# Kernel tuning notes

Hardware: AMD Instinct MI355X
Metric: run time of the kernel (lower is better)

Reference implementation:

```python
import jax, jax.numpy as jnp
import numpy as np

H = 256  # hidden size (hardcoded in module)
F_IN = 10  # input features (hardcoded via x.view(..., 10))


def _lstm_cell(x, h, c, w_ih, w_hh, b_ih, b_hh):
    # PyTorch gate order: i, f, g, o. gates: [B, 4H]
    gates = x @ w_ih.T + h @ w_hh.T + b_ih + b_hh
    i, f, g, o = jnp.split(gates, 4, axis=-1)
    c_new = jax.nn.sigmoid(f) * c + jax.nn.sigmoid(i) * jnp.tanh(g)
    h_new = jax.nn.sigmoid(o) * jnp.tanh(c_new)
    return h_new, c_new


def setup_inputs() -> dict:
    key = jax.random.key(0)
    ks = jax.random.split(key, 13)
    B, T = 512, 1024
    s = 0.05
    return {
        "x": jax.random.normal(ks[0], (B, T, F_IN), dtype=jnp.float32),
        "w_ih0": jax.random.normal(ks[1], (4 * H, F_IN), dtype=jnp.float32) * s,
        "w_hh0": jax.random.normal(ks[2], (4 * H, H), dtype=jnp.float32) * s,
        "b_ih0": jax.random.normal(ks[3], (4 * H,), dtype=jnp.float32) * s,
        "b_hh0": jax.random.normal(ks[4], (4 * H,), dtype=jnp.float32) * s,
        "w_ih1": jax.random.normal(ks[5], (4 * H, H), dtype=jnp.float32) * s,
        "w_hh1": jax.random.normal(ks[6], (4 * H, H), dtype=jnp.float32) * s,
        "b_ih1": jax.random.normal(ks[7], (4 * H,), dtype=jnp.float32) * s,
        "b_hh1": jax.random.normal(ks[8], (4 * H,), dtype=jnp.float32) * s,
        "adv_w1": jax.random.normal(ks[9], (H, H), dtype=jnp.float32) * s,
        "adv_b1": jax.random.normal(ks[10], (H,), dtype=jnp.float32) * s,
        "adv_w2": jax.random.normal(ks[11], (1, H), dtype=jnp.float32) * s,
        "adv_b2": jax.random.normal(ks[12], (1,), dtype=jnp.float32) * s,
    }


def reference(x, w_ih0, w_hh0, b_ih0, b_hh0, w_ih1, w_hh1, b_ih1, b_hh1,
              adv_w1, adv_b1, adv_w2, adv_b2):
    B, T, _ = x.shape
    h0 = jnp.zeros((B, H), dtype=x.dtype)

    def step(carry, x_t):
        h1, c1, h2, c2 = carry
        h1, c1 = _lstm_cell(x_t, h1, c1, w_ih0, w_hh0, b_ih0, b_hh0)
        h2, c2 = _lstm_cell(h1, h2, c2, w_ih1, w_hh1, b_ih1, b_hh1)
        return (h1, c1, h2, c2), h2

    xs = jnp.swapaxes(x, 0, 1)  # [T, B, F_IN]
    _, hs = jax.lax.scan(step, (h0, h0, h0, h0), xs)  # hs: [T, B, H]

    # advantage MLP head applied per-timestep
    hidden = jax.nn.relu(jnp.einsum('tbh,oh->tbo', hs, adv_w1) + adv_b1)
    scores = jnp.einsum('tbh,oh->tbo', hidden, adv_w2) + adv_b2  # [T, B, 1]

    # Faithful to torch.cat(outputs).view(B, -1): flatten TIME-major, then
    # reinterpret as [B, T] (mixes batch and time when B != T).
    flat = scores.reshape(-1)            # time-major flat buffer [T*B]
    mixed = flat.reshape(B, T)
    advantage = jax.nn.softmax(mixed, axis=1)
    return advantage.reshape(-1)
```

## Files before the change

### kernel.cpp

```cpp
#include <hip/hip_runtime.h>
#include <cstdint>
#include <cstddef>

#define Tn 1024
#define Bn 512
#define Hn 256

#define H1S 264
#define H2S 264
#define WHS 264
#define GWS 20

#define H1_OFF  0
#define H2_OFF  (H1_OFF + 32*H1S*2)
#define XB_OFF  (H2_OFF + 32*H2S*2)
#define WH_OFF  (XB_OFF + 2*32*16*2)
#define GW_OFF  (WH_OFF + 16*WHS*2)
#define B1_OFF  (GW_OFF + 8*16*GWS*4)
#define B2_OFF  (B1_OFF + 64*4)
#define BH_OFF  (B2_OFF + 64*4)
#define W2H_OFF (BH_OFF + 16*4)
#define LDS_TOTAL 90112

#define SCORES_OFF 0
#define H1G_OFF  (2*1024*1024)
#define H2G_OFF  (3*1024*1024)
#define FLAG_OFF (4*1024*1024)
#define WS_USED  (4*1024*1024 + 8192)

typedef _Float16 v4h __attribute__((ext_vector_type(4)));
typedef float    v4f __attribute__((ext_vector_type(4)));
typedef unsigned int u32x4 __attribute__((ext_vector_type(4)));
typedef unsigned long long u64;

__device__ inline float sigm(float x){ return 1.0f/(1.0f + __expf(-x)); }
__device__ inline float tanh_f(float x){ return 1.0f - 2.0f/(1.0f + __expf(2.0f*x)); }

__device__ inline v4h cvt4(float4 a){
    v4h f; f[0]=(_Float16)a.x; f[1]=(_Float16)a.y; f[2]=(_Float16)a.z; f[3]=(_Float16)a.w;
    return f;
}

__device__ inline void poll64(const int* tags, int tgt){
    int idx = threadIdx.x & 63;
    while (true){
        int t = __hip_atomic_load(&tags[idx], __ATOMIC_RELAXED, __HIP_MEMORY_SCOPE_AGENT);
        if (__ballot(t < tgt) == 0ull) break;
        __builtin_amdgcn_s_sleep(1);
    }
}

#define LADDR(oo) ( (size_t)(((oo)>>9)*528 + ((oo)&511)) )
__device__ __forceinline__ void stage_tile(const char* gbase, char* lbase, int t){
    u32x4 q0,q1,q2,q3;
    const char* p0 = gbase + t*16;
    const char* p1 = p0 + 4096;
    const char* p2 = p0 + 8192;
    const char* p3 = p0 + 12288;
    asm volatile("global_load_dwordx4 %0, %1, off sc0 sc1" : "=v"(q0) : "v"(p0));
    asm volatile("global_load_dwordx4 %0, %1, off sc0 sc1" : "=v"(q1) : "v"(p1));
    asm volatile("global_load_dwordx4 %0, %1, off sc0 sc1" : "=v"(q2) : "v"(p2));
    asm volatile("global_load_dwordx4 %0, %1, off sc0 sc1" : "=v"(q3) : "v"(p3));
    asm volatile("s_waitcnt vmcnt(0)"
                 : "+v"(q0), "+v"(q1), "+v"(q2), "+v"(q3) :: "memory");
    const int o = t*16;
    *(u32x4*)(lbase + LADDR(o))         = q0;
    *(u32x4*)(lbase + LADDR(o + 4096))  = q1;
    *(u32x4*)(lbase + LADDR(o + 8192))  = q2;
    *(u32x4*)(lbase + LADDR(o + 12288)) = q3;
}

__device__ __forceinline__ void lstm_ew_publish(v4f acc, float* gw, const float* bs,
                                                int n, float& c, _Float16* dst,
                                                int ln15, int ln4)
{
    #pragma unroll
    for (int r = 0; r < 4; ++r) gw[(ln4*4 + r)*GWS + ln15] = acc[r];
    asm volatile("s_waitcnt lgkmcnt(0)" ::: "memory");
    v4f g4 = *(const v4f*)(gw + ln15*GWS + ln4*4);
    asm volatile("s_waitcnt lgkmcnt(0)" ::: "memory");
    v4f bb = *(const v4f*)(bs + n*16 + ln4*4);
    float gi = sigm(g4.x + bb.x), gf = sigm(g4.y + bb.y);
    float gg = tanh_f(g4.z + bb.z), go = sigm(g4.w + bb.w);
    c = gf*c + gi*gg;
    float hn = go * tanh_f(c);
    union { _Float16 h; unsigned short u; } cvt; cvt.h = (_Float16)hn;
    unsigned v32 = cvt.u;
    unsigned p16 = (unsigned)__shfl_xor((int)v32, 16, 64);
    unsigned lo32 = v32 | (p16 << 16);
    unsigned hi32 = (unsigned)__shfl_xor((int)lo32, 32, 64);
    if (ln4 == 0){
        u64 pk = (u64)lo32 | ((u64)hi32 << 32);
        __hip_atomic_store((u64*)dst, pk, __ATOMIC_RELAXED, __HIP_MEMORY_SCOPE_AGENT);
    }
}

__global__ __launch_bounds__(512)
void lstm_pipe(const float* __restrict__ x,
               const float* __restrict__ w_ih0, const float* __restrict__ w_hh0,
               const float* __restrict__ b_ih0, const float* __restrict__ b_hh0,
               const float* __restrict__ w_ih1, const float* __restrict__ w_hh1,
               const float* __restrict__ b_ih1, const float* __restrict__ b_hh1,
               const float* __restrict__ adv_w1, const float* __restrict__ adv_b1,
               const float* __restrict__ adv_w2,
               float* __restrict__ scores, _Float16* __restrict__ h1g,
               _Float16* __restrict__ h2g, int* __restrict__ flags)
{
    extern __shared__ char smem[];
    _Float16* H1l = (_Float16*)(smem + H1_OFF);
    _Float16* H2l = (_Float16*)(smem + H2_OFF);
    _Float16* XBp = (_Float16*)(smem + XB_OFF);
    _Float16* WHl = (_Float16*)(smem + WH_OFF);
    float* gatesc = (float*)(smem + GW_OFF);
    float* b1s    = (float*)(smem + B1_OFF);
    float* b2s    = (float*)(smem + B2_OFF);
    float* bhs    = (float*)(smem + BH_OFF);
    float* w2hs   = (float*)(smem + W2H_OFF);

    const int tid  = threadIdx.x;
    const int lane = tid & 63;
    const int wv   = tid >> 6;
    const int ln15 = lane & 15;
    const int ln4  = lane >> 4;
    const int rt = blockIdx.x >> 4;
    const int us = blockIdx.x & 15;
    const int r0 = rt * 32;
    const int u0 = us * 16;
    const int eng = wv >> 2;
    const int wq  = wv & 3;
    const int m   = wq >> 1;
    const int n0  = (wq & 1) * 2;

    int* tags1 = flags;
    int* tags2 = flags + 1024;

    const int N0i = n0*16 + ln15;
    const int R0 = (N0i & 3)*256 + u0 + (N0i >> 2);
    const int N1i = N0i + 16;
    const int R1 = (N1i & 3)*256 + u0 + (N1i >> 2);
    v4h W[64];
    if (eng == 0){
        #pragma unroll
        for (int t = 0; t < 2; ++t){
            const int R = t ? R1 : R0;
            v4h f;
            #pragma unroll
            for (int j = 0; j < 4; ++j){
                int c = ln4*4 + j;
                f[j] = (_Float16)((c < 10) ? w_ih0[R*10 + c] : 0.f);
            }
            W[t] = f;
        }
        #pragma unroll
        for (int k = 0; k < 16; ++k){
            float4 a0 = *(const float4*)(w_hh0 + (size_t)R0*256 + k*16 + ln4*4);
            float4 a1 = *(const float4*)(w_hh0 + (size_t)R1*256 + k*16 + ln4*4);
            W[2+k]  = cvt4(a0);
            W[18+k] = cvt4(a1);
        }
    } else {
        #pragma unroll
        for (int k = 0; k < 16; ++k){
            float4 a0 = *(const float4*)(w_ih1 + (size_t)R0*256 + k*16 + ln4*4);
            float4 a1 = *(const float4*)(w_ih1 + (size_t)R1*256 + k*16 + ln4*4);
            float4 b0 = *(const float4*)(w_hh1 + (size_t)R0*256 + k*16 + ln4*4);
            float4 b1 = *(const float4*)(w_hh1 + (size_t)R1*256 + k*16 + ln4*4);
            W[k]    = cvt4(a0);
            W[16+k] = cvt4(a1);
            W[32+k] = cvt4(b0);
            W[48+k] = cvt4(b1);
        }
    }

    for (int idx = tid; idx < 16*WHS; idx += 512){
        int n = idx / WHS, c = idx - n*WHS;
        float v = (c < 256) ? adv_w1[(u0+n)*256 + c] : 0.f;
        WHl[idx] = (_Float16)v;
    }
    if (tid < 64){
        int R = (tid & 3)*256 + u0 + (tid >> 2);
        b1s[tid] = b_ih0[R] + b_hh0[R];
        b2s[tid] = b_ih1[R] + b_hh1[R];
    }
    if (tid < 16){
        bhs[tid]  = adv_b1[u0 + tid];
        w2hs[tid] = adv_w2[u0 + tid];
    }
    for (int idx = tid; idx < 1024; idx += 512) XBp[idx] = (_Float16)0.f;
    __syncthreads();
    if (tid < 32){
        const float* xp = x + ((size_t)(r0 + tid)*Tn + 0)*10;
        #pragma unroll
        for (int i = 0; i < 10; ++i) XBp[tid*16 + i] = (_Float16)xp[i];
    }
    __syncthreads();

    float ca = 0.f, cb = 0.f;
    float* gw = gatesc + wv*(16*GWS);

    for (int tau = 0; tau <= Tn + 1; ++tau){
        float xr[10];
        if (wv == 6 && lane < 32 && tau + 1 < Tn){
            const float* xp = x + ((size_t)(r0 + lane)*Tn + (tau+1))*10;
            #pragma unroll
            for (int i = 0; i < 10; ++i) xr[i] = xp[i];
        }
        if (wv == 0 && tau >= 1 && tau <= Tn) poll64(tags1 + rt*64, tau);
        if (wv == 4 && tau >= 2)              poll64(tags2 + rt*64, tau - 1);
        asm volatile("" ::: "memory");
        __syncthreads();

        if (eng == 0){
            if (tau <= Tn){
                const int slot = (tau + 3) & 3;
                stage_tile((const char*)(h1g + (size_t)slot*(Bn*Hn) + (size_t)r0*Hn),
                           (char*)H1l, tid);
            }
        } else {
            if (tau >= 1){
                const int slot = (tau + 2) & 3;
                stage_tile((const char*)(h2g + (size_t)slot*(Bn*Hn) + (size_t)r0*Hn),
                           (char*)H2l, tid - 256);
            }
        }
        __syncthreads();

        if (eng == 0){
            if (tau < Tn){
                v4f acc0 = {0.f,0.f,0.f,0.f}, acc1 = {0.f,0.f,0.f,0.f};
                {
                    v4h a = *(const v4h*)(XBp + (tau & 1)*512 + (m*16 + ln15)*16 + ln4*4);
                    acc0 = __builtin_amdgcn_mfma_f32_16x16x16f16(a, W[0], acc0, 0,0,0);
                    acc1 = __builtin_amdgcn_mfma_f32_16x16x16f16(a, W[1], acc1, 0,0,0);
                }
                const _Float16* Ap = H1l + (m*16 + ln15)*H1S + ln4*4;
                #pragma unroll
                for (int k = 0; k < 16; ++k){
                    v4h a = *(const v4h*)(Ap + k*16);
                    acc0 = __builtin_amdgcn_mfma_f32_16x16x16f16(a, W[2+k],  acc0, 0,0,0);
                    acc1 = __builtin_amdgcn_mfma_f32_16x16x16f16(a, W[18+k], acc1, 0,0,0);
                }
                _Float16* d0 = h1g + (size_t)(tau & 3)*(Bn*Hn)
                             + (size_t)(r0 + m*16 + ln15)*Hn + u0 + n0*4;
                lstm_ew_publish(acc0, gw, b1s, n0,   ca, d0,     ln15, ln4);
                lstm_ew_publish(acc1, gw, b1s, n0+1, cb, d0 + 4, ln15, ln4);
                asm volatile("s_waitcnt vmcnt(0)" ::: "memory");
                if (lane == 0)
                    __hip_atomic_store(&tags1[rt*64 + us*4 + wq], tau + 1,
                                       __ATOMIC_RELAXED, __HIP_MEMORY_SCOPE_AGENT);
            }
        } else {
            if (wv == 6 && lane < 32 && tau + 1 < Tn){
                _Float16* xd = XBp + ((tau+1) & 1)*512 + lane*16;
                #pragma unroll
                for (int i = 0; i < 10; ++i) xd[i] = (_Float16)xr[i];
            }
            if (tau >= 1 && tau <= Tn){
                v4f acc0 = {0.f,0.f,0.f,0.f}, acc1 = {0.f,0.f,0.f,0.f};
                const _Float16* Ap1 = H1l + (m*16 + ln15)*H1S + ln4*4;
                const _Float16* Ap2 = H2l + (m*16 + ln15)*H2S + ln4*4;
                #pragma unroll
                for (int k = 0; k < 16; ++k){
                    v4h a = *(const v4h*)(Ap1 + k*16);
                    acc0 = __builtin_amdgcn_mfma_f32_16x16x16f16(a, W[k],    acc0, 0,0,0);
                    acc1 = __builtin_amdgcn_mfma_f32_16x16x16f16(a, W[16+k], acc1, 0,0,0);
                }
                #pragma unroll
                for (int k = 0; k < 16; ++k){
                    v4h a = *(const v4h*)(Ap2 + k*16);
                    acc0 = __builtin_amdgcn_mfma_f32_16x16x16f16(a, W[32+k], acc0, 0,0,0);
                    acc1 = __builtin_amdgcn_mfma_f32_16x16x16f16(a, W[48+k], acc1, 0,0,0);
                }
                _Float16* d0 = h2g + (size_t)((tau + 3) & 3)*(Bn*Hn)
                             + (size_t)(r0 + m*16 + ln15)*Hn + u0 + n0*4;
                lstm_ew_publish(acc0, gw, b2s, n0,   ca, d0,     ln15, ln4);
                lstm_ew_publish(acc1, gw, b2s, n0+1, cb, d0 + 4, ln15, ln4);
                asm volatile("s_waitcnt vmcnt(0)" ::: "memory");
                if (lane == 0)
                    __hip_atomic_store(&tags2[rt*64 + us*4 + wq], tau,
                                       __ATOMIC_RELAXED, __HIP_MEMORY_SCOPE_AGENT);
            }
            if ((wv == 4 || wv == 5) && tau >= 2){
                const int mh = wv & 1;
                v4f acc = {0.f,0.f,0.f,0.f};
                const _Float16* Ap = H2l + (mh*16 + ln15)*H2S + ln4*4;
                const _Float16* Bp = WHl + ln15*WHS + ln4*4;
                #pragma unroll
                for (int k = 0; k < 16; ++k)
                    acc = __builtin_amdgcn_mfma_f32_16x16x16f16(*(const v4h*)(Ap + k*16),
                                                                *(const v4h*)(Bp + k*16), acc, 0, 0, 0);
                float bh = bhs[ln15], w2 = w2hs[ln15];
                float t0 = fmaxf(acc[0] + bh, 0.f) * w2;
                float t1 = fmaxf(acc[1] + bh, 0.f) * w2;
                float t2 = fmaxf(acc[2] + bh, 0.f) * w2;
                float t3 = fmaxf(acc[3] + bh, 0.f) * w2;
                #pragma unroll
                for (int mk = 1; mk <= 8; mk <<= 1){
                    t0 += __shfl_xor(t0, mk, 64);
                    t1 += __shfl_xor(t1, mk, 64);
                    t2 += __shfl_xor(t2, mk, 64);
                    t3 += __shfl_xor(t3, mk, 64);
                }
                if (ln15 == 0){
                    float* sp = scores + (size_t)(tau - 2)*Bn + r0 + mh*16 + ln4*4;
                    atomicAdd(sp + 0, t0);
                    atomicAdd(sp + 1, t1);
                    atomicAdd(sp + 2, t2);
                    atomicAdd(sp + 3, t3);
                }
            }
        }
        __syncthreads();
    }
}

__global__ __launch_bounds__(256)
void softmax_adv(const float* __restrict__ scores, float* __restrict__ out)
{
    const int b = blockIdx.x, tid = threadIdx.x;
    const int lane = tid & 63, wv = tid >> 6;
    __shared__ float red[4];
    const float4* sp = (const float4*)(scores + (size_t)b*1024);
    float4 v = sp[tid];
    float m = fmaxf(fmaxf(v.x, v.y), fmaxf(v.z, v.w));
    #pragma unroll
    for (int o = 32; o > 0; o >>= 1) m = fmaxf(m, __shfl_xor(m, o, 64));
    if (lane == 0) red[wv] = m;
    __syncthreads();
    m = fmaxf(fmaxf(red[0], red[1]), fmaxf(red[2], red[3]));
    __syncthreads();
    float e0 = __expf(v.x - m), e1 = __expf(v.y - m);
    float e2 = __expf(v.z - m), e3 = __expf(v.w - m);
    float s = e0 + e1 + e2 + e3;
    #pragma unroll
    for (int o = 32; o > 0; o >>= 1) s += __shfl_xor(s, o, 64);
    if (lane == 0) red[wv] = s;
    __syncthreads();
    s = red[0] + red[1] + red[2] + red[3];
    float inv = 1.0f / s;
    float4 o4; o4.x = e0*inv; o4.y = e1*inv; o4.z = e2*inv; o4.w = e3*inv;
    ((float4*)(out + (size_t)b*1024))[tid] = o4;
}

extern "C" void kernel_launch(void* const* d_in, const int* in_sizes, int n_in,
                              void* d_out, int out_size, void* d_ws, size_t ws_size,
                              hipStream_t stream)
{
    (void)in_sizes; (void)n_in; (void)out_size; (void)ws_size;
    const float* x      = (const float*)d_in[0];
    const float* w_ih0  = (const float*)d_in[1];
    const float* w_hh0  = (const float*)d_in[2];
    const float* b_ih0  = (const float*)d_in[3];
    const float* b_hh0  = (const float*)d_in[4];
    const float* w_ih1  = (const float*)d_in[5];
    const float* w_hh1  = (const float*)d_in[6];
    const float* b_ih1  = (const float*)d_in[7];
    const float* b_hh1  = (const float*)d_in[8];
    const float* adv_w1 = (const float*)d_in[9];
    const float* adv_b1 = (const float*)d_in[10];
    const float* adv_w2 = (const float*)d_in[11];

    float*    scores = (float*)((char*)d_ws + SCORES_OFF);
    _Float16* h1g    = (_Float16*)((char*)d_ws + H1G_OFF);
    _Float16* h2g    = (_Float16*)((char*)d_ws + H2G_OFF);
    int*      flags  = (int*)((char*)d_ws + FLAG_OFF);

    hipMemsetAsync(d_ws, 0, WS_USED, stream);
    hipFuncSetAttribute((const void*)lstm_pipe,
                        hipFuncAttributeMaxDynamicSharedMemorySize, LDS_TOTAL);

    hipLaunchKernelGGL(lstm_pipe, dim3(256), dim3(512), LDS_TOTAL, stream,
                       x, w_ih0, w_hh0, b_ih0, b_hh0, w_ih1, w_hh1, b_ih1, b_hh1,
                       adv_w1, adv_b1, adv_w2, scores, h1g, h2g, flags);
    hipLaunchKernelGGL(softmax_adv, dim3(512), dim3(256), 0, stream,
                       scores, (float*)d_out);
}
```

Before: 4.367 ms.

## Split LSTM pipeline into 512 half-size blocks of 16 rows, add poll timeout

Each block now handles 16 batch rows instead of 32, so there are 512 blocks of 256 threads instead of 256 blocks of 512, and each block polls 32 tags instead of 64. The goal is to spread the recurrent work over more CUs with less state to stage per block. A bounded poll with an LDS dead flag lets blocks exit rather than spin forever if not all blocks are co-resident. In exchange, each block loads full weight fragments for half as many rows, the number of cross-block flag syncs doubles, and early exit could silently skip work.

```diff
diff --git a/kernel.cpp b/kernel.cpp
--- a/kernel.cpp
+++ b/kernel.cpp
@@ -12,15 +12,16 @@
 #define GWS 20
 
 #define H1_OFF  0
-#define H2_OFF  (H1_OFF + 32*H1S*2)
-#define XB_OFF  (H2_OFF + 32*H2S*2)
-#define WH_OFF  (XB_OFF + 2*32*16*2)
+#define H2_OFF  (H1_OFF + 16*H1S*2)
+#define XB_OFF  (H2_OFF + 16*H2S*2)
+#define WH_OFF  (XB_OFF + 2*16*16*2)
 #define GW_OFF  (WH_OFF + 16*WHS*2)
-#define B1_OFF  (GW_OFF + 8*16*GWS*4)
+#define B1_OFF  (GW_OFF + 4*16*GWS*4)
 #define B2_OFF  (B1_OFF + 64*4)
 #define BH_OFF  (B2_OFF + 64*4)
 #define W2H_OFF (BH_OFF + 16*4)
-#define LDS_TOTAL 90112
+#define DEAD_OFF (W2H_OFF + 16*4)
+#define LDS_TOTAL 79872
 
 #define SCORES_OFF 0
 #define H1G_OFF  (2*1024*1024)
@@ -28,6 +29,8 @@
 #define FLAG_OFF (4*1024*1024)
 #define WS_USED  (4*1024*1024 + 8192)
 
+#define POLL_GUARD (1 << 22)
+
 typedef _Float16 v4h __attribute__((ext_vector_type(4)));
 typedef float    v4f __attribute__((ext_vector_type(4)));
 typedef unsigned int u32x4 __attribute__((ext_vector_type(4)));
@@ -41,22 +44,24 @@
     return f;
 }
 
-__device__ inline void poll64(const int* tags, int tgt){
-    int idx = threadIdx.x & 63;
+__device__ inline bool poll32(const int* tags, int tgt){
+    int idx = threadIdx.x & 31;
+    int guard = 0;
     while (true){
         int t = __hip_atomic_load(&tags[idx], __ATOMIC_RELAXED, __HIP_MEMORY_SCOPE_AGENT);
-        if (__ballot(t < tgt) == 0ull) break;
+        if (__ballot(t < tgt) == 0ull) return true;
+        if (++guard > POLL_GUARD) return false;
         __builtin_amdgcn_s_sleep(1);
     }
 }
 
 #define LADDR(oo) ( (size_t)(((oo)>>9)*528 + ((oo)&511)) )
-__device__ __forceinline__ void stage_tile(const char* gbase, char* lbase, int t){
+__device__ __forceinline__ void stage_tile8(const char* gbase, char* lbase, int t){
     u32x4 q0,q1,q2,q3;
     const char* p0 = gbase + t*16;
-    const char* p1 = p0 + 4096;
-    const char* p2 = p0 + 8192;
-    const char* p3 = p0 + 12288;
+    const char* p1 = p0 + 2048;
+    const char* p2 = p0 + 4096;
+    const char* p3 = p0 + 6144;
     asm volatile("global_load_dwordx4 %0, %1, off sc0 sc1" : "=v"(q0) : "v"(p0));
     asm volatile("global_load_dwordx4 %0, %1, off sc0 sc1" : "=v"(q1) : "v"(p1));
     asm volatile("global_load_dwordx4 %0, %1, off sc0 sc1" : "=v"(q2) : "v"(p2));
@@ -64,10 +69,10 @@
     asm volatile("s_waitcnt vmcnt(0)"
                  : "+v"(q0), "+v"(q1), "+v"(q2), "+v"(q3) :: "memory");
     const int o = t*16;
-    *(u32x4*)(lbase + LADDR(o))         = q0;
-    *(u32x4*)(lbase + LADDR(o + 4096))  = q1;
-    *(u32x4*)(lbase + LADDR(o + 8192))  = q2;
-    *(u32x4*)(lbase + LADDR(o + 12288)) = q3;
+    *(u32x4*)(lbase + LADDR(o))        = q0;
+    *(u32x4*)(lbase + LADDR(o + 2048)) = q1;
+    *(u32x4*)(lbase + LADDR(o + 4096)) = q2;
+    *(u32x4*)(lbase + LADDR(o + 6144)) = q3;
 }
 
 __device__ __forceinline__ void lstm_ew_publish(v4f acc, float* gw, const float* bs,
@@ -95,7 +100,7 @@
     }
 }
 
-__global__ __launch_bounds__(512)
+__global__ __launch_bounds__(256)
 void lstm_pipe(const float* __restrict__ x,
                const float* __restrict__ w_ih0, const float* __restrict__ w_hh0,
                const float* __restrict__ b_ih0, const float* __restrict__ b_hh0,
@@ -116,6 +121,7 @@
     float* b2s    = (float*)(smem + B2_OFF);
     float* bhs    = (float*)(smem + BH_OFF);
     float* w2hs   = (float*)(smem + W2H_OFF);
+    volatile int* deadp = (volatile int*)(smem + DEAD_OFF);
 
     const int tid  = threadIdx.x;
     const int lane = tid & 63;
@@ -124,15 +130,16 @@
     const int ln4  = lane >> 4;
     const int rt = blockIdx.x >> 4;
     const int us = blockIdx.x & 15;
-    const int r0 = rt * 32;
+    const int r0 = rt * 16;
     const int u0 = us * 16;
-    const int eng = wv >> 2;
-    const int wq  = wv & 3;
-    const int m   = wq >> 1;
-    const int n0  = (wq & 1) * 2;
+    const int eng = wv >> 1;
+    const int wq  = wv & 1;
+    const int n0  = wq * 2;
 
     int* tags1 = flags;
     int* tags2 = flags + 1024;
+
+    if (tid == 0) *deadp = 0;
 
     const int N0i = n0*16 + ln15;
     const int R0 = (N0i & 3)*256 + u0 + (N0i >> 2);
@@ -172,7 +179,7 @@
         }
     }
 
-    for (int idx = tid; idx < 16*WHS; idx += 512){
+    for (int idx = tid; idx < 16*WHS; idx += 256){
         int n = idx / WHS, c = idx - n*WHS;
         float v = (c < 256) ? adv_w1[(u0+n)*256 + c] : 0.f;
         WHl[idx] = (_Float16)v;
@@ -186,9 +193,9 @@
         bhs[tid]  = adv_b1[u0 + tid];
         w2hs[tid] = adv_w2[u0 + tid];
     }
-    for (int idx = tid; idx < 1024; idx += 512) XBp[idx] = (_Float16)0.f;
-    __syncthreads();
-    if (tid < 32){
+    for (int idx = tid; idx < 512; idx += 256) XBp[idx] = (_Float16)0.f;
+    __syncthreads();
+    if (tid < 16){
         const float* xp = x + ((size_t)(r0 + tid)*Tn + 0)*10;
         #pragma unroll
         for (int i = 0; i < 10; ++i) XBp[tid*16 + i] = (_Float16)xp[i];
@@ -200,27 +207,32 @@
 
     for (int tau = 0; tau <= Tn + 1; ++tau){
         float xr[10];
-        if (wv == 6 && lane < 32 && tau + 1 < Tn){
+        if (wv == 3 && lane < 16 && tau + 1 < Tn){
             const float* xp = x + ((size_t)(r0 + lane)*Tn + (tau+1))*10;
             #pragma unroll
             for (int i = 0; i < 10; ++i) xr[i] = xp[i];
         }
-        if (wv == 0 && tau >= 1 && tau <= Tn) poll64(tags1 + rt*64, tau);
-        if (wv == 4 && tau >= 2)              poll64(tags2 + rt*64, tau - 1);
+        if (wv == 0 && tau >= 1 && tau <= Tn){
+            if (!poll32(tags1 + rt*32, tau) && lane == 0) *deadp = 1;
+        }
+        if (wv == 2 && tau >= 2){
+            if (!poll32(tags2 + rt*32, tau - 1) && lane == 0) *deadp = 1;
+        }
         asm volatile("" ::: "memory");
         __syncthreads();
+        if (*deadp) return;
 
         if (eng == 0){
             if (tau <= Tn){
                 const int slot = (tau + 3) & 3;
-                stage_tile((const char*)(h1g + (size_t)slot*(Bn*Hn) + (size_t)r0*Hn),
-                           (char*)H1l, tid);
+                stage_tile8((const char*)(h1g + (size_t)slot*(Bn*Hn) + (size_t)r0*Hn),
+                            (char*)H1l, tid);
             }
         } else {
             if (tau >= 1){
                 const int slot = (tau + 2) & 3;
-                stage_tile((const char*)(h2g + (size_t)slot*(Bn*Hn) + (size_t)r0*Hn),
-                           (char*)H2l, tid - 256);
+                stage_tile8((const char*)(h2g + (size_t)slot*(Bn*Hn) + (size_t)r0*Hn),
+                            (char*)H2l, tid - 128);
             }
         }
         __syncthreads();
@@ -229,11 +241,11 @@
             if (tau < Tn){
                 v4f acc0 = {0.f,0.f,0.f,0.f}, acc1 = {0.f,0.f,0.f,0.f};
                 {
-                    v4h a = *(const v4h*)(XBp + (tau & 1)*512 + (m*16 + ln15)*16 + ln4*4);
+                    v4h a = *(const v4h*)(XBp + (tau & 1)*256 + ln15*16 + ln4*4);
                     acc0 = __builtin_amdgcn_mfma_f32_16x16x16f16(a, W[0], acc0, 0,0,0);
                     acc1 = __builtin_amdgcn_mfma_f32_16x16x16f16(a, W[1], acc1, 0,0,0);
                 }
-                const _Float16* Ap = H1l + (m*16 + ln15)*H1S + ln4*4;
+                const _Float16* Ap = H1l + ln15*H1S + ln4*4;
                 #pragma unroll
                 for (int k = 0; k < 16; ++k){
                     v4h a = *(const v4h*)(Ap + k*16);
@@ -241,24 +253,24 @@
                     acc1 = __builtin_amdgcn_mfma_f32_16x16x16f16(a, W[18+k], acc1, 0,0,0);
                 }
                 _Float16* d0 = h1g + (size_t)(tau & 3)*(Bn*Hn)
-                             + (size_t)(r0 + m*16 + ln15)*Hn + u0 + n0*4;
+                             + (size_t)(r0 + ln15)*Hn + u0 + n0*4;
                 lstm_ew_publish(acc0, gw, b1s, n0,   ca, d0,     ln15, ln4);
                 lstm_ew_publish(acc1, gw, b1s, n0+1, cb, d0 + 4, ln15, ln4);
                 asm volatile("s_waitcnt vmcnt(0)" ::: "memory");
                 if (lane == 0)
-                    __hip_atomic_store(&tags1[rt*64 + us*4 + wq], tau + 1,
+                    __hip_atomic_store(&tags1[rt*32 + us*2 + wq], tau + 1,
                                        __ATOMIC_RELAXED, __HIP_MEMORY_SCOPE_AGENT);
             }
         } else {
-            if (wv == 6 && lane < 32 && tau + 1 < Tn){
-                _Float16* xd = XBp + ((tau+1) & 1)*512 + lane*16;
+            if (wv == 3 && lane < 16 && tau + 1 < Tn){
+                _Float16* xd = XBp + ((tau+1) & 1)*256 + lane*16;
                 #pragma unroll
                 for (int i = 0; i < 10; ++i) xd[i] = (_Float16)xr[i];
             }
             if (tau >= 1 && tau <= Tn){
                 v4f acc0 = {0.f,0.f,0.f,0.f}, acc1 = {0.f,0.f,0.f,0.f};
-                const _Float16* Ap1 = H1l + (m*16 + ln15)*H1S + ln4*4;
-                const _Float16* Ap2 = H2l + (m*16 + ln15)*H2S + ln4*4;
+                const _Float16* Ap1 = H1l + ln15*H1S + ln4*4;
+                const _Float16* Ap2 = H2l + ln15*H2S + ln4*4;
                 #pragma unroll
                 for (int k = 0; k < 16; ++k){
                     v4h a = *(const v4h*)(Ap1 + k*16);
@@ -272,18 +284,17 @@
                     acc1 = __builtin_amdgcn_mfma_f32_16x16x16f16(a, W[48+k], acc1, 0,0,0);
                 }
                 _Float16* d0 = h2g + (size_t)((tau + 3) & 3)*(Bn*Hn)
-                             + (size_t)(r0 + m*16 + ln15)*Hn + u0 + n0*4;
+                             + (size_t)(r0 + ln15)*Hn + u0 + n0*4;
                 lstm_ew_publish(acc0, gw, b2s, n0,   ca, d0,     ln15, ln4);
                 lstm_ew_publish(acc1, gw, b2s, n0+1, cb, d0 + 4, ln15, ln4);
                 asm volatile("s_waitcnt vmcnt(0)" ::: "memory");
                 if (lane == 0)
-                    __hip_atomic_store(&tags2[rt*64 + us*4 + wq], tau,
+                    __hip_atomic_store(&tags2[rt*32 + us*2 + wq], tau,
                                        __ATOMIC_RELAXED, __HIP_MEMORY_SCOPE_AGENT);
             }
-            if ((wv == 4 || wv == 5) && tau >= 2){
-                const int mh = wv & 1;
+            if (wv == 2 && tau >= 2){
                 v4f acc = {0.f,0.f,0.f,0.f};
-                const _Float16* Ap = H2l + (mh*16 + ln15)*H2S + ln4*4;
+                const _Float16* Ap = H2l + ln15*H2S + ln4*4;
                 const _Float16* Bp = WHl + ln15*WHS + ln4*4;
                 #pragma unroll
                 for (int k = 0; k < 16; ++k)
@@ -302,7 +313,7 @@
                     t3 += __shfl_xor(t3, mk, 64);
                 }
                 if (ln15 == 0){
-                    float* sp = scores + (size_t)(tau - 2)*Bn + r0 + mh*16 + ln4*4;
+                    float* sp = scores + (size_t)(tau - 2)*Bn + r0 + ln4*4;
                     atomicAdd(sp + 0, t0);
                     atomicAdd(sp + 1, t1);
                     atomicAdd(sp + 2, t2);
@@ -369,7 +380,7 @@
     hipFuncSetAttribute((const void*)lstm_pipe,
                         hipFuncAttributeMaxDynamicSharedMemorySize, LDS_TOTAL);
 
-    hipLaunchKernelGGL(lstm_pipe, dim3(256), dim3(512), LDS_TOTAL, stream,
+    hipLaunchKernelGGL(lstm_pipe, dim3(512), dim3(256), LDS_TOTAL, stream,
                        x, w_ih0, w_hh0, b_ih0, b_hh0, w_ih1, w_hh1, b_ih1, b_hh1,
                        adv_w1, adv_b1, adv_w2, scores, h1g, h2g, flags);
     hipLaunchKernelGGL(softmax_adv, dim3(512), dim3(256), 0, stream,
```

Measured after the change: 3.924 ms. 10.1% less time.
